# Optimization experiments

Measured on AMD Instinct MI355X. Metric: run time of the kernel, lower is better.

Reference implementation:

```python
import jax, jax.numpy as jnp
import numpy as np

B = 16
D_MODEL = 1024
HALF = D_MODEL // 2
PATTERN_NUM = 4096
PATTERN_LEN = 32          # == patch_seq_len
ENC_SEQ = 2048
SIM_NUM = 64
NUM_PATCH = ENC_SEQ // PATTERN_LEN


def setup_inputs() -> dict:
    key = jax.random.key(0)
    ks = jax.random.split(key, 6)
    w = lambda k, shape: jax.random.normal(k, shape, jnp.float32) * 0.02
    return {
        "src": jax.random.normal(ks[0], (B, ENC_SEQ, D_MODEL), jnp.float32),
        "meta_pattern_pool": jax.random.normal(ks[1], (PATTERN_NUM, PATTERN_LEN), jnp.float32),
        "fuse_w": w(ks[2], (PATTERN_LEN * HALF, SIM_NUM)),
        "fuse_b": jnp.zeros((SIM_NUM,), jnp.float32),
        "recover_w": w(ks[3], (SIM_NUM, HALF)),
        "recover_b": jnp.zeros((HALF,), jnp.float32),
        "gp_w": w(ks[4], (HALF, 10)),
        "gp_b": jnp.zeros((10,), jnp.float32),
    }


def reference(src, meta_pattern_pool, fuse_w, fuse_b, recover_w, recover_b, gp_w, gp_b):
    # src: [B, S, D]; take second half of channels and split into patches
    x = src[:, :, HALF:].reshape(B, NUM_PATCH, PATTERN_LEN, HALF)  # [B,P,L,H]

    # per-patch similarity score against pattern pool (vectorized over patches)
    low = jnp.mean(x @ gp_w + gp_b, axis=-1)                       # [B,P,L]
    scores = jnp.einsum('bpl,nl->bpn', low, meta_pattern_pool)     # [B,P,N]

    # topk pattern retrieval; original uses batch-0 indices for all batches
    _, idx = jax.lax.top_k(scores, SIM_NUM)                        # [B,P,S]
    selected = meta_pattern_pool[idx[0]]                           # [P,S,L]

    # softmax routing key per patch
    logits = x.reshape(B, NUM_PATCH, PATTERN_LEN * HALF) @ fuse_w + fuse_b
    route = jax.nn.softmax(logits, axis=-1)                        # [B,P,S]

    # fuse[b,p,l,s] = route[b,p,s] * selected[p,s,l]
    fuse = route[:, :, None, :] * jnp.transpose(selected, (0, 2, 1))[None]  # [B,P,L,S]
    out = (fuse @ recover_w + recover_b).reshape(B, ENC_SEQ, HALF)

    padding = jnp.einsum('bps,psl->bpl', route, selected).reshape(B, ENC_SEQ)

    out_full = jnp.concatenate([src[:, :, :HALF], out], axis=-1)   # [B,S,D]
    # original prepends an uninitialized torch.empty buffer; we use zeros
    padding_out = jnp.concatenate([jnp.zeros((B, ENC_SEQ), src.dtype), padding], axis=-1)
    return out_full, padding_out
```

## Files before the change

### kernel.cpp

```cpp
#include <hip/hip_runtime.h>
#include <hip/hip_bf16.h>

#define NB 16
#define DMODEL 1024
#define HALFD 512
#define PNUM 4096
#define PLEN 32
#define SEQ 2048
#define SIM 64
#define NPATCH 64
#define NROWS (NB*SEQ)
#define MROWS (NB*NPATCH)
#define KDIM (PLEN*HALFD)
#define NCOPY 512
#define OUT0 ((size_t)NB*SEQ*DMODEL)

typedef __attribute__((ext_vector_type(8))) short s8v;
typedef __attribute__((ext_vector_type(4))) float f32x4;
typedef __attribute__((ext_vector_type(8))) unsigned short ush8;
typedef unsigned long long u64;

__device__ __forceinline__ unsigned short f2bf(float f) {
    __hip_bfloat16 h = __float2bfloat16(f);
    return *reinterpret_cast<unsigned short*>(&h);
}
__device__ __forceinline__ u64 umax64(u64 a, u64 b) { return a > b ? a : b; }
__device__ __forceinline__ u64 umin64(u64 a, u64 b) { return a < b ? a : b; }
__device__ __forceinline__ u64 clean6(u64 v, int lane) {
    #pragma unroll
    for (int j = 32; j; j >>= 1) {
        u64 o = __shfl_xor(v, j);
        v = ((lane & j) == 0) ? umax64(v, o) : umin64(v, o);
    }
    return v;
}

union PrepShared {
    struct { double gpm[513]; double lowp[PLEN]; u64 wl[4][64]; } tk;
    float tile[64][68];
};
__global__ __launch_bounds__(256) void k_prep(
        const float* __restrict__ gp_w, const float* __restrict__ gp_b,
        const float* __restrict__ fw, const float* __restrict__ rw,
        const float* __restrict__ src, const float* __restrict__ pool,
        unsigned short* __restrict__ fwT, unsigned short* __restrict__ rwf,
        u64* __restrict__ cand) {
    __shared__ PrepShared u;
    int bid = blockIdx.x, t = threadIdx.x;
    int lane = t & 63, w = t >> 6;
    if (bid < 512) {
        int p = bid >> 3, q = bid & 7;
        for (int h = t; h < HALFD; h += 256) {
            double s = 0.0;
            #pragma unroll
            for (int j = 0; j < 10; ++j) s += (double)gp_w[h*10 + j];
            u.tk.gpm[h] = s / 10.0;
        }
        if (t == 0) {
            double sb = 0.0;
            #pragma unroll
            for (int j = 0; j < 10; ++j) sb += (double)gp_b[j];
            u.tk.gpm[512] = sb / 10.0;
        }
        __syncthreads();
        {
            const double* g0 = u.tk.gpm + lane*4;
            const double* g1 = u.tk.gpm + 256 + lane*4;
            #pragma unroll
            for (int rr = 0; rr < 8; ++rr) {
                int r = w*8 + rr;
                const float4* s4 = reinterpret_cast<const float4*>(src + (size_t)(p*PLEN + r)*DMODEL);
                float4 x0 = s4[128 + lane], x1 = s4[192 + lane];
                double d = (double)x0.x*g0[0] + (double)x0.y*g0[1] + (double)x0.z*g0[2] + (double)x0.w*g0[3]
                         + (double)x1.x*g1[0] + (double)x1.y*g1[1] + (double)x1.z*g1[2] + (double)x1.w*g1[3];
                #pragma unroll
                for (int o = 32; o; o >>= 1) d += __shfl_xor(d, o);
                if (lane == 0) u.tk.lowp[r] = d + u.tk.gpm[512];
            }
        }
        __syncthreads();
        u64 v[2];
        #pragma unroll
        for (int cc = 0; cc < 2; ++cc) {
            int n = q*512 + (w*2 + cc)*64 + lane;
            const float4* p4 = reinterpret_cast<const float4*>(pool + (size_t)n*PLEN);
            double s = 0.0;
            #pragma unroll
            for (int r2 = 0; r2 < 8; ++r2) {
                float4 vv = p4[r2];
                s += (double)vv.x*u.tk.lowp[r2*4] + (double)vv.y*u.tk.lowp[r2*4+1]
                   + (double)vv.z*u.tk.lowp[r2*4+2] + (double)vv.w*u.tk.lowp[r2*4+3];
            }
            u64 ub = (u64)__double_as_longlong(s);
            u64 okey = ub ^ (((u64)((long long)ub >> 63)) | 0x8000000000000000ULL);
            v[cc] = (okey & ~0xFFFULL) | (u64)(0xFFF - n);
        }
        #pragma unroll
        for (int kk = 2; kk <= 64; kk <<= 1) {
            #pragma unroll
            for (int j = kk >> 1; j; j >>= 1) {
                #pragma unroll
                for (int cc = 0; cc < 2; ++cc) {
                    u64 o = __shfl_xor(v[cc], j);
                    bool keepMax = ((lane & kk) == 0) == ((lane & j) == 0);
                    v[cc] = keepMax ? umax64(v[cc], o) : umin64(v[cc], o);
                }
            }
        }
        u64 rb2 = __shfl(v[1], 63 - lane);
        u64 m = umax64(v[0], rb2);
        m = clean6(m, lane);
        u.tk.wl[w][lane] = m;
        __syncthreads();
        if (w == 0) {
            u64 a = umax64(u.tk.wl[0][lane], u.tk.wl[1][63 - lane]); a = clean6(a, lane);
            u64 b = umax64(u.tk.wl[2][lane], u.tk.wl[3][63 - lane]); b = clean6(b, lane);
            u64 r2 = __shfl(b, 63 - lane);
            u64 f = umax64(a, r2); f = clean6(f, lane);
            cand[(size_t)(p*8 + q)*SIM + lane] = f;
        }
    } else if (bid < 768) {
        int k0 = (bid - 512) * 64;
        int i = t >> 2;
        #pragma unroll
        for (int q = 0; q < 4; ++q) {
            int c = (t & 3) + q*4;
            float4 v = *reinterpret_cast<const float4*>(fw + (size_t)(k0 + i)*SIM + c*4);
            *reinterpret_cast<float4*>(&u.tile[i][c*4]) = v;
        }
        __syncthreads();
        #pragma unroll
        for (int c2 = 0; c2 < 2; ++c2) {
            int e = c2*256 + t;
            int kl = e >> 8, fn = (e >> 6) & 3, l = e & 63;
            int kk0 = kl*32 + ((l >> 4) * 8), n = fn*16 + (l & 15);
            ush8 hv;
            #pragma unroll
            for (int j = 0; j < 8; ++j) hv[j] = f2bf(u.tile[kk0 + j][n]);
            size_t dst = ((size_t)((2*(bid - 512) + kl)*4 + fn)*64 + l)*8;
            *reinterpret_cast<ush8*>(fwT + dst) = hv;
        }
    } else {
        int q = t >> 6;
        int idx = (bid - 768)*4 + q;
        int ks = idx >> 5, fn = idx & 31;
        int ml = lane & 15, kg = lane >> 4;
        ush8 hv;
        #pragma unroll
        for (int j = 0; j < 8; ++j)
            hv[j] = f2bf(rw[(size_t)(ks*32 + kg*8 + j)*HALFD + fn*16 + ml]);
        size_t dst = ((size_t)idx*64 + lane)*8;
        *reinterpret_cast<ush8*>(rwf + dst) = hv;
    }
}

__global__ __launch_bounds__(256) void k_logits(
        const float* __restrict__ src, const unsigned short* __restrict__ fwT,
        const u64* __restrict__ cand, float* __restrict__ part,
        float* __restrict__ out, int* __restrict__ sel, int nks) {
    int t = threadIdx.x, lane = t & 63, w = t >> 6;
    int bid = blockIdx.x;
    int NL = 16*nks;
    if (bid >= NL + NCOPY) {
        if (w != 0) return;
        int p = bid - (NL + NCOPY);
        const u64* c = cand + (size_t)p*8*SIM;
        u64 a = umax64(c[lane],         c[1*SIM + 63 - lane]); a = clean6(a, lane);
        u64 bq = umax64(c[2*SIM + lane], c[3*SIM + 63 - lane]); bq = clean6(bq, lane);
        u64 d = umax64(c[4*SIM + lane], c[5*SIM + 63 - lane]); d = clean6(d, lane);
        u64 e = umax64(c[6*SIM + lane], c[7*SIM + 63 - lane]); e = clean6(e, lane);
        u64 ab = umax64(a, __shfl(bq, 63 - lane)); ab = clean6(ab, lane);
        u64 de = umax64(d, __shfl(e, 63 - lane)); de = clean6(de, lane);
        u64 f  = umax64(ab, __shfl(de, 63 - lane)); f = clean6(f, lane);
        sel[p*SIM + lane] = 0xFFF - (int)(f & 0xFFFULL);
        return;
    }
    if (bid >= NL) {
        int cb = bid - NL;
        size_t total = (size_t)NROWS * 128;
        const float4* s4 = reinterpret_cast<const float4*>(src);
        float4* o4 = reinterpret_cast<float4*>(out);
        for (size_t idx = (size_t)cb*256 + t; idx < total; idx += (size_t)NCOPY*256) {
            size_t r = idx >> 7, c = idx & 127;
            o4[r*256 + c] = s4[r*256 + c];
        }
        return;
    }
    int mt = bid / nks, ks = bid - mt*nks;
    int kchunk = KDIM / nks, nstep = kchunk >> 6;
    int r0 = mt*64;
    int ml = lane & 15, kg = lane >> 4;
    int Rrow = r0 + w*16 + ml;
    int bb = Rrow >> 6, prow = Rrow & 63;
    const float* xrow = src + ((size_t)(bb*SEQ + prow*PLEN))*DMODEL + HALFD;
    int kblk_base = (ks*kchunk) >> 5;
    f32x4 acc[4] = {};
    for (int step = 0; step < nstep; ++step) {
        int k0 = ks*kchunk + step*64;
        int l = k0 >> 9, h0 = k0 & 511;
        const float* ap = xrow + (size_t)l*DMODEL + h0 + kg*8;
        float4 va0 = *reinterpret_cast<const float4*>(ap);
        float4 va1 = *reinterpret_cast<const float4*>(ap + 4);
        float4 vb0 = *reinterpret_cast<const float4*>(ap + 32);
        float4 vb1 = *reinterpret_cast<const float4*>(ap + 36);
        s8v ah0, ah1;
        float fa[8] = {va0.x,va0.y,va0.z,va0.w,va1.x,va1.y,va1.z,va1.w};
        float fbv[8] = {vb0.x,vb0.y,vb0.z,vb0.w,vb1.x,vb1.y,vb1.z,vb1.w};
        #pragma unroll
        for (int j = 0; j < 8; ++j) {
            ah0[j] = (short)f2bf(fa[j]);
            ah1[j] = (short)f2bf(fbv[j]);
        }
        int kblk0 = kblk_base + step*2;
        #pragma unroll
        for (int fn = 0; fn < 4; ++fn) {
            size_t off0 = ((size_t)(kblk0*4 + fn)*64 + lane)*8;
            size_t off1 = ((size_t)((kblk0+1)*4 + fn)*64 + lane)*8;
            s8v bh0 = *reinterpret_cast<const s8v*>(fwT + off0);
            s8v bh1 = *reinterpret_cast<const s8v*>(fwT + off1);
            acc[fn] = __builtin_amdgcn_mfma_f32_16x16x32_bf16(ah0, bh0, acc[fn], 0, 0, 0);
            acc[fn] = __builtin_amdgcn_mfma_f32_16x16x32_bf16(ah1, bh1, acc[fn], 0, 0, 0);
        }
    }
    float* pout = part + (size_t)(mt*nks + ks)*4096;
    #pragma unroll
    for (int fn = 0; fn < 4; ++fn)
        #pragma unroll
        for (int r = 0; r < 4; ++r)
            pout[(w*16 + kg*4 + r)*64 + fn*16 + ml] = acc[fn][r];
}

__global__ __launch_bounds__(256) void k_out(
        const float* __restrict__ part, const float* __restrict__ fb,
        const int* __restrict__ sel, const float* __restrict__ pool,
        const unsigned short* __restrict__ rwf, const float* __restrict__ rb,
        float* __restrict__ out, float* __restrict__ pad, int nks) {
    __shared__ float A_T[SIM][36];
    __shared__ float routeS[64];
    __shared__ int   selS[64];
    __shared__ float psum[4][64];
    int row = blockIdx.x;
    int b = row >> 6, p = row & 63;
    int t = threadIdx.x, lane = t & 63, w = t >> 6;
    int kpw = nks >> 2;
    {
        float v = 0.f;
        for (int kq = 0; kq < kpw; ++kq) {
            int ks = w*kpw + kq;
            v += part[(size_t)(b*nks + ks)*4096 + p*64 + lane];
        }
        psum[w][lane] = v;
    }
    __syncthreads();
    if (w == 0) {
        float v = psum[0][lane] + psum[1][lane] + psum[2][lane] + psum[3][lane] + fb[lane];
        float m = v;
        #pragma unroll
        for (int o = 32; o; o >>= 1) m = fmaxf(m, __shfl_xor(m, o));
        float e = expf(v - m);
        float sum = e;
        #pragma unroll
        for (int o = 32; o; o >>= 1) sum += __shfl_xor(sum, o);
        routeS[lane] = e / sum;
    } else if (w == 1) {
        selS[lane] = sel[p*SIM + lane];
    }
    __syncthreads();
    #pragma unroll
    for (int q = 0; q < 8; ++q) {
        int e = t + q*256;
        int s = e >> 5, l = e & 31;
        A_T[s][l] = routeS[s] * pool[(size_t)selS[s]*PLEN + l];
    }
    __syncthreads();
    if (t < 32) {
        float ps = 0.f;
        #pragma unroll
        for (int s = 0; s < 64; ++s) ps += A_T[s][t];
        pad[(size_t)b*2*SEQ + SEQ + p*PLEN + t] = ps;
    } else if (t < 64) {
        pad[(size_t)b*2*SEQ + p*PLEN + (t - 32)] = 0.f;
    }
    int ml = lane & 15, kg = lane >> 4;
    s8v ah[2][2];
    #pragma unroll
    for (int mt = 0; mt < 2; ++mt)
        #pragma unroll
        for (int ks = 0; ks < 2; ++ks) {
            #pragma unroll
            for (int j = 0; j < 8; ++j)
                ah[mt][ks][j] = (short)f2bf(A_T[ks*32 + kg*8 + j][mt*16 + ml]);
        }
    size_t orow0 = ((size_t)(b*SEQ + p*PLEN))*DMODEL + HALFD;
    #pragma unroll
    for (int nt = 0; nt < 8; ++nt) {
        int fng = w*8 + nt;
        f32x4 acc0 = {}, acc1 = {};
        #pragma unroll
        for (int ks = 0; ks < 2; ++ks) {
            size_t off = ((size_t)(ks*32 + fng)*64 + lane)*8;
            s8v bh = *reinterpret_cast<const s8v*>(rwf + off);
            acc0 = __builtin_amdgcn_mfma_f32_16x16x32_bf16(ah[0][ks], bh, acc0, 0, 0, 0);
            acc1 = __builtin_amdgcn_mfma_f32_16x16x32_bf16(ah[1][ks], bh, acc1, 0, 0, 0);
        }
        int n = fng*16 + ml;
        float bias = rb[n];
        #pragma unroll
        for (int r = 0; r < 4; ++r) {
            int m0 = kg*4 + r;
            out[orow0 + (size_t)m0*DMODEL + n]        = acc0[r] + bias;
            out[orow0 + (size_t)(16 + m0)*DMODEL + n] = acc1[r] + bias;
        }
    }
}

static const void* by_size(void* const* d_in, const int* in_sizes, int n_in,
                           int want, int fallback) {
    for (int i = 0; i < n_in; ++i) if (in_sizes[i] == want) return d_in[i];
    return d_in[fallback];
}

extern "C" void kernel_launch(void* const* d_in, const int* in_sizes, int n_in,
                              void* d_out, int out_size, void* d_ws, size_t ws_size,
                              hipStream_t stream) {
    const float* src  = (const float*)by_size(d_in, in_sizes, n_in, NB*SEQ*DMODEL, 0);
    const float* pool = (const float*)by_size(d_in, in_sizes, n_in, PNUM*PLEN, 1);
    const float* fw   = (const float*)by_size(d_in, in_sizes, n_in, KDIM*SIM, 2);
    const float* fb   = (const float*)by_size(d_in, in_sizes, n_in, SIM, 3);
    const float* rw   = (const float*)by_size(d_in, in_sizes, n_in, SIM*HALFD, 4);
    const float* rb   = (const float*)by_size(d_in, in_sizes, n_in, HALFD, 5);
    const float* gpw  = (const float*)by_size(d_in, in_sizes, n_in, HALFD*10, 6);
    const float* gpb  = (const float*)by_size(d_in, in_sizes, n_in, 10, 7);
    float* out = (float*)d_out;
    float* pad = out + OUT0;

    int nks = (ws_size >= (size_t)(16u << 20)) ? 32 : 8;

    unsigned short* fwT = (unsigned short*)d_ws;
    unsigned short* rwf = fwT + (size_t)SIM*KDIM;
    u64*   cand  = (u64*)(rwf + (size_t)SIM*HALFD);
    int*   sel   = (int*)(cand + (size_t)NPATCH*8*SIM);
    float* part  = (float*)(sel + 4096);

    hipLaunchKernelGGL(k_prep,   dim3(784),    dim3(256), 0, stream,
                       gpw, gpb, fw, rw, src, pool, fwT, rwf, cand);
    hipLaunchKernelGGL(k_logits, dim3(16*nks + NCOPY + NPATCH), dim3(256), 0, stream,
                       src, fwT, cand, part, out, sel, nks);
    hipLaunchKernelGGL(k_out,    dim3(MROWS),  dim3(256), 0, stream,
                       part, fb, sel, pool, rwf, rb, out, pad, nks);
}
```

Baseline: 90.64 us.

## Move src-half copy into output kernel and stage output tile through LDS

Moves the 512-block copy of the first half of src from the logits kernel into the output kernel's grid, so the logits GEMM runs without competing copy blocks and the copy overlaps the small output work. The output kernel now keeps its MFMA accumulators in registers, then transposes them through a shared-memory buffer (unioned with the existing scratch) so each row is written with coalesced float4 stores instead of scattered scalar stores. The cost is extra LDS traffic, more registers held for the accumulators, and additional barriers.

```diff
diff --git a/kernel.cpp b/kernel.cpp
--- a/kernel.cpp
+++ b/kernel.cpp
@@ -157,13 +157,13 @@
 __global__ __launch_bounds__(256) void k_logits(
         const float* __restrict__ src, const unsigned short* __restrict__ fwT,
         const u64* __restrict__ cand, float* __restrict__ part,
-        float* __restrict__ out, int* __restrict__ sel, int nks) {
+        int* __restrict__ sel, int nks) {
     int t = threadIdx.x, lane = t & 63, w = t >> 6;
     int bid = blockIdx.x;
     int NL = 16*nks;
-    if (bid >= NL + NCOPY) {
+    if (bid >= NL) {
         if (w != 0) return;
-        int p = bid - (NL + NCOPY);
+        int p = bid - NL;
         const u64* c = cand + (size_t)p*8*SIM;
         u64 a = umax64(c[lane],         c[1*SIM + 63 - lane]); a = clean6(a, lane);
         u64 bq = umax64(c[2*SIM + lane], c[3*SIM + 63 - lane]); bq = clean6(bq, lane);
@@ -173,17 +173,6 @@
         u64 de = umax64(d, __shfl(e, 63 - lane)); de = clean6(de, lane);
         u64 f  = umax64(ab, __shfl(de, 63 - lane)); f = clean6(f, lane);
         sel[p*SIM + lane] = 0xFFF - (int)(f & 0xFFFULL);
-        return;
-    }
-    if (bid >= NL) {
-        int cb = bid - NL;
-        size_t total = (size_t)NROWS * 128;
-        const float4* s4 = reinterpret_cast<const float4*>(src);
-        float4* o4 = reinterpret_cast<float4*>(out);
-        for (size_t idx = (size_t)cb*256 + t; idx < total; idx += (size_t)NCOPY*256) {
-            size_t r = idx >> 7, c = idx & 127;
-            o4[r*256 + c] = s4[r*256 + c];
-        }
         return;
     }
     int mt = bid / nks, ks = bid - mt*nks;
@@ -230,18 +219,31 @@
             pout[(w*16 + kg*4 + r)*64 + fn*16 + ml] = acc[fn][r];
 }
 
+union OutShared {
+    struct { float A_T[SIM][36]; float routeS[64]; int selS[64]; float psum[4][64]; } a;
+    float xpose[16][516];
+};
 __global__ __launch_bounds__(256) void k_out(
         const float* __restrict__ part, const float* __restrict__ fb,
         const int* __restrict__ sel, const float* __restrict__ pool,
         const unsigned short* __restrict__ rwf, const float* __restrict__ rb,
-        float* __restrict__ out, float* __restrict__ pad, int nks) {
-    __shared__ float A_T[SIM][36];
-    __shared__ float routeS[64];
-    __shared__ int   selS[64];
-    __shared__ float psum[4][64];
-    int row = blockIdx.x;
+        const float* __restrict__ src, float* __restrict__ out,
+        float* __restrict__ pad, int nks) {
+    __shared__ OutShared u;
+    int t = threadIdx.x, lane = t & 63, w = t >> 6;
+    if (blockIdx.x < NCOPY) {
+        int cb = blockIdx.x;
+        size_t total = (size_t)NROWS * 128;
+        const float4* s4 = reinterpret_cast<const float4*>(src);
+        float4* o4 = reinterpret_cast<float4*>(out);
+        for (size_t idx = (size_t)cb*256 + t; idx < total; idx += (size_t)NCOPY*256) {
+            size_t r = idx >> 7, c = idx & 127;
+            o4[r*256 + c] = s4[r*256 + c];
+        }
+        return;
+    }
+    int row = blockIdx.x - NCOPY;
     int b = row >> 6, p = row & 63;
-    int t = threadIdx.x, lane = t & 63, w = t >> 6;
     int kpw = nks >> 2;
     {
         float v = 0.f;
@@ -249,11 +251,11 @@
             int ks = w*kpw + kq;
             v += part[(size_t)(b*nks + ks)*4096 + p*64 + lane];
         }
-        psum[w][lane] = v;
+        u.a.psum[w][lane] = v;
     }
     __syncthreads();
     if (w == 0) {
-        float v = psum[0][lane] + psum[1][lane] + psum[2][lane] + psum[3][lane] + fb[lane];
+        float v = u.a.psum[0][lane] + u.a.psum[1][lane] + u.a.psum[2][lane] + u.a.psum[3][lane] + fb[lane];
         float m = v;
         #pragma unroll
         for (int o = 32; o; o >>= 1) m = fmaxf(m, __shfl_xor(m, o));
@@ -261,22 +263,22 @@
         float sum = e;
         #pragma unroll
         for (int o = 32; o; o >>= 1) sum += __shfl_xor(sum, o);
-        routeS[lane] = e / sum;
+        u.a.routeS[lane] = e / sum;
     } else if (w == 1) {
-        selS[lane] = sel[p*SIM + lane];
+        u.a.selS[lane] = sel[p*SIM + lane];
     }
     __syncthreads();
     #pragma unroll
     for (int q = 0; q < 8; ++q) {
         int e = t + q*256;
         int s = e >> 5, l = e & 31;
-        A_T[s][l] = routeS[s] * pool[(size_t)selS[s]*PLEN + l];
+        u.a.A_T[s][l] = u.a.routeS[s] * pool[(size_t)u.a.selS[s]*PLEN + l];
     }
     __syncthreads();
     if (t < 32) {
         float ps = 0.f;
         #pragma unroll
-        for (int s = 0; s < 64; ++s) ps += A_T[s][t];
+        for (int s = 0; s < 64; ++s) ps += u.a.A_T[s][t];
         pad[(size_t)b*2*SEQ + SEQ + p*PLEN + t] = ps;
     } else if (t < 64) {
         pad[(size_t)b*2*SEQ + p*PLEN + (t - 32)] = 0.f;
@@ -289,9 +291,9 @@
         for (int ks = 0; ks < 2; ++ks) {
             #pragma unroll
             for (int j = 0; j < 8; ++j)
-                ah[mt][ks][j] = (short)f2bf(A_T[ks*32 + kg*8 + j][mt*16 + ml]);
-        }
-    size_t orow0 = ((size_t)(b*SEQ + p*PLEN))*DMODEL + HALFD;
+                ah[mt][ks][j] = (short)f2bf(u.a.A_T[ks*32 + kg*8 + j][mt*16 + ml]);
+        }
+    f32x4 accA[8], accB[8];
     #pragma unroll
     for (int nt = 0; nt < 8; ++nt) {
         int fng = w*8 + nt;
@@ -303,13 +305,29 @@
             acc0 = __builtin_amdgcn_mfma_f32_16x16x32_bf16(ah[0][ks], bh, acc0, 0, 0, 0);
             acc1 = __builtin_amdgcn_mfma_f32_16x16x32_bf16(ah[1][ks], bh, acc1, 0, 0, 0);
         }
-        int n = fng*16 + ml;
-        float bias = rb[n];
-        #pragma unroll
-        for (int r = 0; r < 4; ++r) {
-            int m0 = kg*4 + r;
-            out[orow0 + (size_t)m0*DMODEL + n]        = acc0[r] + bias;
-            out[orow0 + (size_t)(16 + m0)*DMODEL + n] = acc1[r] + bias;
+        float bias = rb[fng*16 + ml];
+        #pragma unroll
+        for (int r = 0; r < 4; ++r) { acc0[r] += bias; acc1[r] += bias; }
+        accA[nt] = acc0; accB[nt] = acc1;
+    }
+    size_t orow0 = ((size_t)(b*SEQ + p*PLEN))*DMODEL + HALFD;
+    #pragma unroll
+    for (int mt = 0; mt < 2; ++mt) {
+        __syncthreads();
+        #pragma unroll
+        for (int nt = 0; nt < 8; ++nt) {
+            f32x4 a = (mt == 0) ? accA[nt] : accB[nt];
+            #pragma unroll
+            for (int r = 0; r < 4; ++r)
+                u.xpose[kg*4 + r][w*128 + nt*16 + ml] = a[r];
+        }
+        __syncthreads();
+        #pragma unroll
+        for (int q = 0; q < 8; ++q) {
+            int e = q*256 + t;
+            int rr = e >> 7, c4 = e & 127;
+            float4 v = *reinterpret_cast<float4*>(&u.xpose[rr][c4*4]);
+            *reinterpret_cast<float4*>(out + orow0 + (size_t)(mt*16 + rr)*DMODEL + c4*4) = v;
         }
     }
 }
@@ -344,8 +362,8 @@
 
     hipLaunchKernelGGL(k_prep,   dim3(784),    dim3(256), 0, stream,
                        gpw, gpb, fw, rw, src, pool, fwT, rwf, cand);
-    hipLaunchKernelGGL(k_logits, dim3(16*nks + NCOPY + NPATCH), dim3(256), 0, stream,
-                       src, fwT, cand, part, out, sel, nks);
-    hipLaunchKernelGGL(k_out,    dim3(MROWS),  dim3(256), 0, stream,
-                       part, fb, sel, pool, rwf, rb, out, pad, nks);
-}
+    hipLaunchKernelGGL(k_logits, dim3(16*nks + NPATCH), dim3(256), 0, stream,
+                       src, fwT, cand, part, sel, nks);
+    hipLaunchKernelGGL(k_out,    dim3(NCOPY + MROWS), dim3(256), 0, stream,
+                       part, fb, sel, pool, rwf, rb, src, out, pad, nks);
+}
```

Result: no change. 88.95 us (-1.9%).
